# Kernel tuning notes

Hardware: AMD Instinct MI355X
Metric: run time of the kernel (lower is better)

Reference implementation:

```python
import jax, jax.numpy as jnp
import numpy as np
import math

B, S, HID, H = 2, 4096, 512, 8
D_K = HID // H


def setup_inputs() -> dict:
    key = jax.random.key(0)
    ks = jax.random.split(key, 8)
    inp = {
        "query": jax.random.normal(ks[0], (B, S, HID), dtype=jnp.float32),
        "key": jax.random.normal(ks[1], (B, S, HID), dtype=jnp.float32),
        "value": jax.random.normal(ks[2], (B, S, HID), dtype=jnp.float32),
        "mask": jax.random.randint(ks[3], (B, S), 0, 2, dtype=jnp.int32),
        # conv1d kernel_size=1, bias=False -> plain [out,in] weights (xavier-normal-ish)
        "Wq": jax.random.normal(ks[4], (HID, HID), dtype=jnp.float32) * (1.0 / math.sqrt(HID)),
        "Wk": jax.random.normal(ks[5], (HID, HID), dtype=jnp.float32) * (1.0 / math.sqrt(HID)),
        "Wv": jax.random.normal(ks[6], (HID, HID), dtype=jnp.float32) * (1.0 / math.sqrt(HID)),
        "Wo": jax.random.normal(ks[7], (HID, HID), dtype=jnp.float32) * (1.0 / math.sqrt(HID)),
    }
    return inp


def reference(query, key, value, mask, Wq, Wk, Wv, Wo):
    b, s, _ = query.shape
    # conv1d(k=1, bias=False) projection == x @ W.T; split heads -> [b,h,s,d_k]
    def proj(x, W):
        return jnp.einsum('bsd,ed->bse', x, W).reshape(b, s, H, D_K).transpose(0, 2, 1, 3)
    q, k, v = proj(query, Wq), proj(key, Wk), proj(value, Wv)
    # NOTE: original scales by 1/log(d_k), not 1/sqrt(d_k)
    score = jnp.einsum('bhqd,bhkd->bhqk', q, k) / math.log(D_K)
    m = mask.reshape(b, 1, 1, s)  # broadcast over heads and query positions
    score = jnp.where(m == 0, jnp.float32(-1e30), score)
    attn = jax.nn.softmax(score, axis=-1)  # dropout is identity in eval
    x = jnp.einsum('bhqk,bhkd->bhqd', attn, v)
    x = x.transpose(0, 2, 1, 3).reshape(b, s, HID)
    return jnp.einsum('bsd,ed->bse', x, Wo)
```

## Files before the change

### kernel.cpp

```cpp
#include <hip/hip_runtime.h>
#include <hip/hip_bf16.h>
#include <cstdint>
#include <cstddef>


namespace {

constexpr int kB = 2, kS = 4096, kHid = 512, kH = 8, kDk = 64;
constexpr int kBH = kB * kH;
constexpr int kM = kB * kS;

typedef __attribute__((ext_vector_type(8))) short short8;
typedef __attribute__((ext_vector_type(4))) float floatx4;
typedef __attribute__((ext_vector_type(16))) float floatx16;
typedef __attribute__((ext_vector_type(4))) unsigned int uintx4;
typedef unsigned short u16;

__device__ __forceinline__ u16 bf16rne(float f) {
    uint32_t u = __float_as_uint(f);
    u += 0x7fffu + ((u >> 16) & 1u);
    return (u16)(u >> 16);
}
__device__ __forceinline__ uint32_t pk2(float lo, float hi) {
#if __has_builtin(__builtin_amdgcn_cvt_pk_bf16_f32)
    typedef __attribute__((ext_vector_type(2))) __bf16 bf2;
    bf2 h = __builtin_amdgcn_cvt_pk_bf16_f32(lo, hi);
    return __builtin_bit_cast(uint32_t, h);
#else
    return ((uint32_t)bf16rne(hi) << 16) | (uint32_t)bf16rne(lo);
#endif
}
__device__ __forceinline__ float fexp2(float x) {
#if __has_builtin(__builtin_amdgcn_exp2f)
    return __builtin_amdgcn_exp2f(x);
#else
    return exp2f(x);
#endif
}
__device__ __forceinline__ float bf2f(u16 v) {
    return __uint_as_float((uint32_t)v << 16);
}
__device__ __forceinline__ void plswap(uint32_t& a, uint32_t& b) {
#if __has_builtin(__builtin_amdgcn_permlane32_swap)
    typedef __attribute__((ext_vector_type(2))) unsigned int uint2v;
    uint2v r = __builtin_amdgcn_permlane32_swap(a, b, false, false);
    a = r[0]; b = r[1];
#else
    asm volatile("v_permlane32_swap_b32 %0, %1" : "+v"(a), "+v"(b));
#endif
}
__device__ __forceinline__ void gload16(const void* g, void* l) {
    __builtin_amdgcn_global_load_lds(
        (const __attribute__((address_space(1))) void*)g,
        (__attribute__((address_space(3))) void*)l, 16, 0, 0);
}

__global__ __launch_bounds__(256) void cvt_qw(const float* __restrict__ q,
    const float* __restrict__ k, const float* __restrict__ v,
    const float* __restrict__ w0, const float* __restrict__ w1,
    const float* __restrict__ w2, const float* __restrict__ w3,
    u16* __restrict__ xall, u16* __restrict__ wall) {
    const int bx = blockIdx.x;
    if (bx < 12288) {
        int z = bx >> 12;
        size_t i = (size_t)(bx & 4095) * 256 + threadIdx.x;
        const float* src = z == 0 ? q : (z == 1 ? k : v);
        float4 f = ((const float4*)src)[i];
        ushort4 o;
        o.x = bf16rne(f.x); o.y = bf16rne(f.y);
        o.z = bf16rne(f.z); o.w = bf16rne(f.w);
        ((ushort4*)(xall + (size_t)z * kM * kHid))[i] = o;
    } else {
        int r = bx - 12288;
        int z = r >> 8;
        size_t i = (size_t)(r & 255) * 256 + threadIdx.x;
        const float* src = z == 0 ? w0 : (z == 1 ? w1 : (z == 2 ? w2 : w3));
        float sc = (z == 0)
            ? (float)(1.4426950408889634 / (6.0 * 0.6931471805599453))
            : 1.0f;
        float4 f = ((const float4*)src)[i];
        ushort4 o;
        o.x = bf16rne(f.x * sc); o.y = bf16rne(f.y * sc);
        o.z = bf16rne(f.z * sc); o.w = bf16rne(f.w * sc);
        ((ushort4*)(wall + (size_t)z * kHid * kHid))[i] = o;
    }
}

__global__ __launch_bounds__(256) void cvt_mask(const int* __restrict__ mask,
    float* __restrict__ fb) {
    int i = blockIdx.x * 256 + threadIdx.x;
    fb[i] = mask[i] ? 0.0f : -1e30f;
}

__global__ __launch_bounds__(256, 3) void proj(const u16* __restrict__ xall,
    const u16* __restrict__ wall, u16* __restrict__ qp, u16* __restrict__ kp,
    u16* __restrict__ vt) {
    __shared__ float smt[4][16][68];
    const int z = blockIdx.z;
    const u16* x = xall + (size_t)z * kM * kHid;
    const u16* w = wall + (size_t)z * kHid * kHid;
    const int wv = threadIdx.x >> 6, lane = threadIdx.x & 63;
    const int quad = lane >> 4, l16 = lane & 15;
    const int mb = blockIdx.y * 128 + (wv >> 1) * 64;
    const int nb = blockIdx.x * 128 + (wv & 1) * 64;
    floatx4 acc[4][4] = {};
    const u16* xr = x + (size_t)(mb + l16) * kHid + quad * 8;
    const u16* wr = w + (size_t)(nb + l16) * kHid + quad * 8;
    for (int k0 = 0; k0 < kHid; k0 += 32) {
        short8 a[4], bt[4];
#pragma unroll
        for (int i = 0; i < 4; i++)
            a[i] = *(const short8*)(xr + (size_t)i * 16 * kHid + k0);
#pragma unroll
        for (int t = 0; t < 4; t++)
            bt[t] = *(const short8*)(wr + (size_t)t * 16 * kHid + k0);
#pragma unroll
        for (int i = 0; i < 4; i++)
#pragma unroll
        for (int t = 0; t < 4; t++)
            acc[i][t] = __builtin_amdgcn_mfma_f32_16x16x32_bf16(a[i], bt[t], acc[i][t], 0, 0, 0);
    }
    if (z < 2) {
        u16* dst = (z == 0) ? qp : kp;
        const int row16 = lane >> 2, cseg = (lane & 3) * 16;
#pragma unroll
        for (int i = 0; i < 4; i++) {
#pragma unroll
            for (int t = 0; t < 4; t++)
#pragma unroll
            for (int r = 0; r < 4; r++)
                smt[wv][quad * 4 + r][t * 16 + l16] = acc[i][t][r];
            __builtin_amdgcn_wave_barrier();
            const float* rp = &smt[wv][row16][cseg];
            float4 f0 = *(const float4*)(rp);
            float4 f1 = *(const float4*)(rp + 4);
            float4 f2 = *(const float4*)(rp + 8);
            float4 f3 = *(const float4*)(rp + 12);
            uint4 o0, o1;
            o0.x = pk2(f0.x, f0.y); o0.y = pk2(f0.z, f0.w);
            o0.z = pk2(f1.x, f1.y); o0.w = pk2(f1.z, f1.w);
            o1.x = pk2(f2.x, f2.y); o1.y = pk2(f2.z, f2.w);
            o1.z = pk2(f3.x, f3.y); o1.w = pk2(f3.z, f3.w);
            u16* dp = dst + (size_t)(mb + i * 16 + row16) * kHid + nb + cseg;
            *(uint4*)dp = o0;
            *(uint4*)(dp + 8) = o1;
            __builtin_amdgcn_wave_barrier();
        }
    } else {
#pragma unroll
        for (int i = 0; i < 4; i++)
#pragma unroll
        for (int t = 0; t < 4; t++) {
            int m0 = mb + i * 16 + quad * 4;
            int n = nb + t * 16 + l16;
            int b = m0 >> 12, s = m0 & (kS - 1);
            int h = n >> 6,   d = n & (kDk - 1);
            ushort4 o;
            o.x = bf16rne(acc[i][t][0]); o.y = bf16rne(acc[i][t][1]);
            o.z = bf16rne(acc[i][t][2]); o.w = bf16rne(acc[i][t][3]);
            *(ushort4*)(vt + ((size_t)(b * kH + h) * kDk + d) * kS + s) = o;
        }
    }
}

__global__ __launch_bounds__(256, 2) void attn(const u16* __restrict__ qp,
    const u16* __restrict__ kp, const u16* __restrict__ vt,
    const float* __restrict__ fbias, u16* __restrict__ ows,
    float* __restrict__ rsws) {
    union SmT {
        struct { u16 K[2][64][64]; u16 V[2][64][64]; } s;
        float ep[4][32][33];
    };
    __shared__ __align__(16) SmT sm;
    const int tid = threadIdx.x;
    const int wv = tid >> 6, l = tid & 63;
    const int hf = l >> 5, q32 = l & 31, l7 = l & 7;
    const int wg = blockIdx.x;
    const int bh = ((wg & 7) << 1) | ((wg >> 3) & 1);
    const int qb = (wg >> 4) & 15;
    const int kz = wg >> 8;
    const int b = bh >> 3, h = bh & 7;
    const int qbase = qb * 256 + wv * 64;
    const u16* Qb = qp + (size_t)b * kS * kHid + h * 64;
    const u16* Kb = kp + (size_t)b * kS * kHid + h * 64;
    const u16* Vb = vt + (size_t)bh * kDk * kS;
    const float* fm = fbias + b * kS;

    short8 qf[2][4];
#pragma unroll
    for (int qt = 0; qt < 2; qt++)
#pragma unroll
    for (int m = 0; m < 4; m++)
        qf[qt][m] = *(const short8*)(Qb + (size_t)(qbase + qt * 32 + q32) * kHid + m * 16 + hf * 8);

    floatx16 O[2][2] = {};
    float rs[2] = {0.0f, 0.0f};

    const int srow = l >> 3;
    const int pcol = (l7 ^ srow) * 8;
    const u16* pK = Kb + (size_t)(kz * 64 + wv * 8 + srow) * kHid + pcol;
    const u16* pV = Vb + (size_t)(wv * 8 + srow) * kS + kz * 64 + pcol;
    auto stage = [&](int ph) {
        gload16(pK,                        &sm.s.K[ph][wv * 8][0]);
        gload16(pK + (size_t)32 * kHid,    &sm.s.K[ph][wv * 8 + 32][0]);
        gload16(pV,                        &sm.s.V[ph][wv * 8][0]);
        gload16(pV + (size_t)32 * kS,      &sm.s.V[ph][wv * 8 + 32][0]);
        pK += (size_t)128 * kHid;
        pV += 128;
    };

    stage(0);
    __syncthreads();

    for (int s5 = 0; s5 < 32; ++s5) {
        const int ph = s5 & 1;
        const int kt = (kz + 2 * s5) * 64;
        if (s5 < 31) stage(ph ^ 1);
#pragma unroll
        for (int ks = 0; ks < 2; ++ks) {
            short8 kf[4];
#pragma unroll
            for (int m = 0; m < 4; m++)
                kf[m] = *(const short8*)&sm.s.K[ph][ks * 32 + q32][((2 * m + hf) ^ l7) * 8];
            short8 vf[2][2];
#pragma unroll
            for (int ds = 0; ds < 2; ds++)
#pragma unroll
            for (int tt = 0; tt < 2; tt++)
                vf[ds][tt] = *(const short8*)&sm.s.V[ph][ds * 32 + q32][((ks * 4 + tt * 2 + hf) ^ l7) * 8];
            const float* fp = fm + kt + ks * 32 + 4 * hf;
            float4 g0 = *(const float4*)(fp);
            float4 g1 = *(const float4*)(fp + 8);
            float4 g2 = *(const float4*)(fp + 16);
            float4 g3 = *(const float4*)(fp + 24);
#pragma unroll
            for (int qt = 0; qt < 2; ++qt) {
                floatx16 st;
                st[0] = g0.x;  st[1] = g0.y;  st[2] = g0.z;  st[3] = g0.w;
                st[4] = g1.x;  st[5] = g1.y;  st[6] = g1.z;  st[7] = g1.w;
                st[8] = g2.x;  st[9] = g2.y;  st[10] = g2.z; st[11] = g2.w;
                st[12] = g3.x; st[13] = g3.y; st[14] = g3.z; st[15] = g3.w;
#pragma unroll
                for (int m = 0; m < 4; m++)
                    st = __builtin_amdgcn_mfma_f32_32x32x16_bf16(kf[m], qf[qt][m], st, 0, 0, 0);
                float xx[16];
#pragma unroll
                for (int r = 0; r < 16; r++) xx[r] = fexp2(st[r]);
                rs[qt] += (((xx[0] + xx[1]) + (xx[2] + xx[3])) + ((xx[4] + xx[5]) + (xx[6] + xx[7])))
                        + (((xx[8] + xx[9]) + (xx[10] + xx[11])) + ((xx[12] + xx[13]) + (xx[14] + xx[15])));
                uint32_t w00 = pk2(xx[0], xx[1]),   w01 = pk2(xx[2], xx[3]);
                uint32_t w10 = pk2(xx[4], xx[5]),   w11 = pk2(xx[6], xx[7]);
                uint32_t w20 = pk2(xx[8], xx[9]),   w21 = pk2(xx[10], xx[11]);
                uint32_t w30 = pk2(xx[12], xx[13]), w31 = pk2(xx[14], xx[15]);
                plswap(w00, w10); plswap(w01, w11);
                plswap(w20, w30); plswap(w21, w31);
                uintx4 t0 = {w00, w01, w10, w11};
                uintx4 t1 = {w20, w21, w30, w31};
                short8 bf0 = __builtin_bit_cast(short8, t0);
                short8 bf1 = __builtin_bit_cast(short8, t1);
                O[qt][0] = __builtin_amdgcn_mfma_f32_32x32x16_bf16(vf[0][0], bf0, O[qt][0], 0, 0, 0);
                O[qt][0] = __builtin_amdgcn_mfma_f32_32x32x16_bf16(vf[0][1], bf1, O[qt][0], 0, 0, 0);
                O[qt][1] = __builtin_amdgcn_mfma_f32_32x32x16_bf16(vf[1][0], bf0, O[qt][1], 0, 0, 0);
                O[qt][1] = __builtin_amdgcn_mfma_f32_32x32x16_bf16(vf[1][1], bf1, O[qt][1], 0, 0, 0);
            }
        }
        __syncthreads();
    }

#pragma unroll
    for (int qt = 0; qt < 2; ++qt) {
        float r = rs[qt];
        r += __shfl_xor(r, 32);
        if (hf == 0)
            rsws[((size_t)kz * kBH + bh) * kS + qbase + qt * 32 + q32] = r;
        u16* Ob = ows + (((size_t)kz * kBH + bh) * kS + qbase + qt * 32) * kDk;
#pragma unroll
        for (int ds = 0; ds < 2; ds++) {
#pragma unroll
            for (int rr = 0; rr < 16; rr++)
                sm.ep[wv][q32][(rr & 3) + 8 * (rr >> 2) + 4 * hf] = O[qt][ds][rr];
            __builtin_amdgcn_wave_barrier();
            {
                const int qq = l >> 1, c0 = (l & 1) * 16;
                float f[16];
#pragma unroll
                for (int j = 0; j < 16; j++) f[j] = sm.ep[wv][qq][c0 + j];
                uint4 o0, o1;
                o0.x = pk2(f[0], f[1]);   o0.y = pk2(f[2], f[3]);
                o0.z = pk2(f[4], f[5]);   o0.w = pk2(f[6], f[7]);
                o1.x = pk2(f[8], f[9]);   o1.y = pk2(f[10], f[11]);
                o1.z = pk2(f[12], f[13]); o1.w = pk2(f[14], f[15]);
                u16* dp = Ob + (size_t)qq * kDk + ds * 32 + c0;
                *(uint4*)dp = o0;
                *(uint4*)(dp + 8) = o1;
            }
            __builtin_amdgcn_wave_barrier();
        }
    }
}

__global__ __launch_bounds__(256) void combine(const u16* __restrict__ ows,
    const float* __restrict__ rsws, u16* __restrict__ xo) {
    size_t i = (size_t)blockIdx.x * 256 + threadIdx.x;
    const int d8 = (int)(i & 7);
    const int s  = (int)((i >> 3) & (kS - 1));
    const int bh = (int)(i >> 15);
    const int b = bh >> 3, h = bh & 7;
    const size_t base = ((size_t)bh * kS + s) * kDk + d8 * 8;
    short8 a = *(const short8*)(ows + base);
    short8 c = *(const short8*)(ows + (size_t)kBH * kS * kDk + base);
    float r = rsws[(size_t)bh * kS + s] + rsws[(size_t)kBH * kS + (size_t)bh * kS + s];
    float inv = 1.0f / r;
    float e[8];
#pragma unroll
    for (int j = 0; j < 8; j++)
        e[j] = (bf2f((u16)a[j]) + bf2f((u16)c[j])) * inv;
    uint4 o;
    o.x = pk2(e[0], e[1]); o.y = pk2(e[2], e[3]);
    o.z = pk2(e[4], e[5]); o.w = pk2(e[6], e[7]);
    *(uint4*)(xo + ((size_t)b * kS + s) * kHid + h * 64 + d8 * 8) = o;
}

__global__ __launch_bounds__(256, 3) void oproj(const u16* __restrict__ x,
    const u16* __restrict__ w, float* __restrict__ out) {
    const int wv = threadIdx.x >> 6, lane = threadIdx.x & 63;
    const int quad = lane >> 4, l16 = lane & 15;
    const int mb = blockIdx.y * 128 + (wv >> 1) * 64;
    const int nb = blockIdx.x * 128 + (wv & 1) * 64;
    floatx4 acc[4][4] = {};
    const u16* xr = x + (size_t)(mb + l16) * kHid + quad * 8;
    const u16* wr = w + (size_t)(nb + l16) * kHid + quad * 8;
    for (int k0 = 0; k0 < kHid; k0 += 32) {
        short8 a[4], bt[4];
#pragma unroll
        for (int i = 0; i < 4; i++)
            a[i] = *(const short8*)(xr + (size_t)i * 16 * kHid + k0);
#pragma unroll
        for (int t = 0; t < 4; t++)
            bt[t] = *(const short8*)(wr + (size_t)t * 16 * kHid + k0);
#pragma unroll
        for (int i = 0; i < 4; i++)
#pragma unroll
        for (int t = 0; t < 4; t++)
            acc[i][t] = __builtin_amdgcn_mfma_f32_16x16x32_bf16(a[i], bt[t], acc[i][t], 0, 0, 0);
    }
#pragma unroll
    for (int i = 0; i < 4; i++)
#pragma unroll
    for (int t = 0; t < 4; t++)
#pragma unroll
    for (int r = 0; r < 4; r++) {
        int m = mb + i * 16 + quad * 4 + r;
        int n = nb + t * 16 + l16;
        out[(size_t)m * kHid + n] = acc[i][t][r];
    }
}

}

extern "C" void kernel_launch(void* const* d_in, const int* in_sizes, int n_in,
                              void* d_out, int out_size, void* d_ws, size_t ws_size,
                              hipStream_t stream) {
    const float* q  = (const float*)d_in[0];
    const float* k  = (const float*)d_in[1];
    const float* v  = (const float*)d_in[2];
    const int* mask = (const int*)d_in[3];
    const float* w0 = (const float*)d_in[4];
    const float* w1 = (const float*)d_in[5];
    const float* w2 = (const float*)d_in[6];
    const float* w3 = (const float*)d_in[7];
    float* out = (float*)d_out;

    u16* ws   = (u16*)d_ws;
    u16* xall = ws;
    u16* wall = xall + (size_t)3 * kM * kHid;
    u16* qp   = wall + (size_t)4 * kHid * kHid;
    u16* kp   = qp + (size_t)kBH * kS * kDk;
    u16* vt   = kp + (size_t)kBH * kS * kDk;
    u16* ows  = xall;
    float* fbias = (float*)(xall + (size_t)2 * kM * kHid);
    float* rsws  = fbias + (size_t)kB * kS;
    u16* xo   = qp;

    dim3 blk(256);
    cvt_qw <<<dim3(13312), blk, 0, stream>>>(q, k, v, w0, w1, w2, w3, xall, wall);
    proj   <<<dim3(kHid / 128, kM / 128, 3), blk, 0, stream>>>(xall, wall, qp, kp, vt);
    cvt_mask<<<dim3(kB * kS / 256), blk, 0, stream>>>(mask, fbias);
    attn   <<<dim3(512), blk, 0, stream>>>(qp, kp, vt, fbias, ows, rsws);
    combine<<<dim3(2048), blk, 0, stream>>>(ows, rsws, xo);
    oproj  <<<dim3(kHid / 128, kM / 128), blk, 0, stream>>>(
        xo, wall + (size_t)3 * kHid * kHid, out);
}
```

Baseline: 264.9 us.

## Fuse fp32-to-bf16 conversion into projections and split attention keys three ways

Drops the standalone conversion kernel. The projection and output-projection GEMMs now read fp32 inputs and weights and convert them to bf16 in registers, and the softmax scale moves to the Q projection epilogue. Attention splits the key range into three partitions instead of two (768 blocks, occupancy hint raised to 3), and combine sums three partial results. This removes one launch and a bf16 round trip through memory, but each GEMM tile now loads twice as many bytes and the extra key split adds partial-output traffic. The mask loads also move inside the qt loop and the row-sum reduction uses packed float2 adds.

```diff
diff --git a/kernel.cpp b/kernel.cpp
--- a/kernel.cpp
+++ b/kernel.cpp
@@ -9,8 +9,10 @@
 constexpr int kB = 2, kS = 4096, kHid = 512, kH = 8, kDk = 64;
 constexpr int kBH = kB * kH;
 constexpr int kM = kB * kS;
+constexpr int kKZ = 3;
 
 typedef __attribute__((ext_vector_type(8))) short short8;
+typedef __attribute__((ext_vector_type(2))) float float2v;
 typedef __attribute__((ext_vector_type(4))) float floatx4;
 typedef __attribute__((ext_vector_type(16))) float floatx16;
 typedef __attribute__((ext_vector_type(4))) unsigned int uintx4;
@@ -54,36 +56,11 @@
         (const __attribute__((address_space(1))) void*)g,
         (__attribute__((address_space(3))) void*)l, 16, 0, 0);
 }
-
-__global__ __launch_bounds__(256) void cvt_qw(const float* __restrict__ q,
-    const float* __restrict__ k, const float* __restrict__ v,
-    const float* __restrict__ w0, const float* __restrict__ w1,
-    const float* __restrict__ w2, const float* __restrict__ w3,
-    u16* __restrict__ xall, u16* __restrict__ wall) {
-    const int bx = blockIdx.x;
-    if (bx < 12288) {
-        int z = bx >> 12;
-        size_t i = (size_t)(bx & 4095) * 256 + threadIdx.x;
-        const float* src = z == 0 ? q : (z == 1 ? k : v);
-        float4 f = ((const float4*)src)[i];
-        ushort4 o;
-        o.x = bf16rne(f.x); o.y = bf16rne(f.y);
-        o.z = bf16rne(f.z); o.w = bf16rne(f.w);
-        ((ushort4*)(xall + (size_t)z * kM * kHid))[i] = o;
-    } else {
-        int r = bx - 12288;
-        int z = r >> 8;
-        size_t i = (size_t)(r & 255) * 256 + threadIdx.x;
-        const float* src = z == 0 ? w0 : (z == 1 ? w1 : (z == 2 ? w2 : w3));
-        float sc = (z == 0)
-            ? (float)(1.4426950408889634 / (6.0 * 0.6931471805599453))
-            : 1.0f;
-        float4 f = ((const float4*)src)[i];
-        ushort4 o;
-        o.x = bf16rne(f.x * sc); o.y = bf16rne(f.y * sc);
-        o.z = bf16rne(f.z * sc); o.w = bf16rne(f.w * sc);
-        ((ushort4*)(wall + (size_t)z * kHid * kHid))[i] = o;
-    }
+__device__ __forceinline__ short8 cvt8(const float* p) {
+    float4 a = *(const float4*)p;
+    float4 b = *(const float4*)(p + 4);
+    uintx4 u = {pk2(a.x, a.y), pk2(a.z, a.w), pk2(b.x, b.y), pk2(b.z, b.w)};
+    return __builtin_bit_cast(short8, u);
 }
 
 __global__ __launch_bounds__(256) void cvt_mask(const int* __restrict__ mask,
@@ -92,28 +69,30 @@
     fb[i] = mask[i] ? 0.0f : -1e30f;
 }
 
-__global__ __launch_bounds__(256, 3) void proj(const u16* __restrict__ xall,
-    const u16* __restrict__ wall, u16* __restrict__ qp, u16* __restrict__ kp,
-    u16* __restrict__ vt) {
+__global__ __launch_bounds__(256, 3) void proj(const float* __restrict__ xq,
+    const float* __restrict__ xk, const float* __restrict__ xv,
+    const float* __restrict__ w0, const float* __restrict__ w1,
+    const float* __restrict__ w2,
+    u16* __restrict__ qp, u16* __restrict__ kp, u16* __restrict__ vt) {
     __shared__ float smt[4][16][68];
     const int z = blockIdx.z;
-    const u16* x = xall + (size_t)z * kM * kHid;
-    const u16* w = wall + (size_t)z * kHid * kHid;
+    const float* x = z == 0 ? xq : (z == 1 ? xk : xv);
+    const float* w = z == 0 ? w0 : (z == 1 ? w1 : w2);
     const int wv = threadIdx.x >> 6, lane = threadIdx.x & 63;
     const int quad = lane >> 4, l16 = lane & 15;
     const int mb = blockIdx.y * 128 + (wv >> 1) * 64;
     const int nb = blockIdx.x * 128 + (wv & 1) * 64;
     floatx4 acc[4][4] = {};
-    const u16* xr = x + (size_t)(mb + l16) * kHid + quad * 8;
-    const u16* wr = w + (size_t)(nb + l16) * kHid + quad * 8;
+    const float* xr = x + (size_t)(mb + l16) * kHid + quad * 8;
+    const float* wr = w + (size_t)(nb + l16) * kHid + quad * 8;
     for (int k0 = 0; k0 < kHid; k0 += 32) {
         short8 a[4], bt[4];
 #pragma unroll
         for (int i = 0; i < 4; i++)
-            a[i] = *(const short8*)(xr + (size_t)i * 16 * kHid + k0);
+            a[i] = cvt8(xr + (size_t)i * 16 * kHid + k0);
 #pragma unroll
         for (int t = 0; t < 4; t++)
-            bt[t] = *(const short8*)(wr + (size_t)t * 16 * kHid + k0);
+            bt[t] = cvt8(wr + (size_t)t * 16 * kHid + k0);
 #pragma unroll
         for (int i = 0; i < 4; i++)
 #pragma unroll
@@ -121,6 +100,8 @@
             acc[i][t] = __builtin_amdgcn_mfma_f32_16x16x32_bf16(a[i], bt[t], acc[i][t], 0, 0, 0);
     }
     if (z < 2) {
+        const float scl = (z == 0)
+            ? (float)(1.4426950408889634 / (6.0 * 0.6931471805599453)) : 1.0f;
         u16* dst = (z == 0) ? qp : kp;
         const int row16 = lane >> 2, cseg = (lane & 3) * 16;
 #pragma unroll
@@ -137,10 +118,10 @@
             float4 f2 = *(const float4*)(rp + 8);
             float4 f3 = *(const float4*)(rp + 12);
             uint4 o0, o1;
-            o0.x = pk2(f0.x, f0.y); o0.y = pk2(f0.z, f0.w);
-            o0.z = pk2(f1.x, f1.y); o0.w = pk2(f1.z, f1.w);
-            o1.x = pk2(f2.x, f2.y); o1.y = pk2(f2.z, f2.w);
-            o1.z = pk2(f3.x, f3.y); o1.w = pk2(f3.z, f3.w);
+            o0.x = pk2(f0.x * scl, f0.y * scl); o0.y = pk2(f0.z * scl, f0.w * scl);
+            o0.z = pk2(f1.x * scl, f1.y * scl); o0.w = pk2(f1.z * scl, f1.w * scl);
+            o1.x = pk2(f2.x * scl, f2.y * scl); o1.y = pk2(f2.z * scl, f2.w * scl);
+            o1.z = pk2(f3.x * scl, f3.y * scl); o1.w = pk2(f3.z * scl, f3.w * scl);
             u16* dp = dst + (size_t)(mb + i * 16 + row16) * kHid + nb + cseg;
             *(uint4*)dp = o0;
             *(uint4*)(dp + 8) = o1;
@@ -163,7 +144,7 @@
     }
 }
 
-__global__ __launch_bounds__(256, 2) void attn(const u16* __restrict__ qp,
+__global__ __launch_bounds__(256, 3) void attn(const u16* __restrict__ qp,
     const u16* __restrict__ kp, const u16* __restrict__ vt,
     const float* __restrict__ fbias, u16* __restrict__ ows,
     float* __restrict__ rsws) {
@@ -176,9 +157,13 @@
     const int wv = tid >> 6, l = tid & 63;
     const int hf = l >> 5, q32 = l & 31, l7 = l & 7;
     const int wg = blockIdx.x;
-    const int bh = ((wg & 7) << 1) | ((wg >> 3) & 1);
-    const int qb = (wg >> 4) & 15;
-    const int kz = wg >> 8;
+    const int xcd = wg & 7;
+    const int widx = wg >> 3;
+    const int bh = (xcd << 1) | (widx & 1);
+    const int rest = widx >> 1;
+    const int qb = rest & 15;
+    const int kz = rest >> 4;
+    const int nt = (kz == 0) ? 22 : 21;
     const int b = bh >> 3, h = bh & 7;
     const int qbase = qb * 256 + wv * 64;
     const u16* Qb = qp + (size_t)b * kS * kHid + h * 64;
@@ -205,17 +190,17 @@
         gload16(pK + (size_t)32 * kHid,    &sm.s.K[ph][wv * 8 + 32][0]);
         gload16(pV,                        &sm.s.V[ph][wv * 8][0]);
         gload16(pV + (size_t)32 * kS,      &sm.s.V[ph][wv * 8 + 32][0]);
-        pK += (size_t)128 * kHid;
-        pV += 128;
+        pK += (size_t)(kKZ * 64) * kHid;
+        pV += kKZ * 64;
     };
 
     stage(0);
     __syncthreads();
 
-    for (int s5 = 0; s5 < 32; ++s5) {
+    for (int s5 = 0; s5 < nt; ++s5) {
         const int ph = s5 & 1;
-        const int kt = (kz + 2 * s5) * 64;
-        if (s5 < 31) stage(ph ^ 1);
+        const int kt = (kz + kKZ * s5) * 64;
+        if (s5 < nt - 1) stage(ph ^ 1);
 #pragma unroll
         for (int ks = 0; ks < 2; ++ks) {
             short8 kf[4];
@@ -229,12 +214,12 @@
             for (int tt = 0; tt < 2; tt++)
                 vf[ds][tt] = *(const short8*)&sm.s.V[ph][ds * 32 + q32][((ks * 4 + tt * 2 + hf) ^ l7) * 8];
             const float* fp = fm + kt + ks * 32 + 4 * hf;
-            float4 g0 = *(const float4*)(fp);
-            float4 g1 = *(const float4*)(fp + 8);
-            float4 g2 = *(const float4*)(fp + 16);
-            float4 g3 = *(const float4*)(fp + 24);
 #pragma unroll
             for (int qt = 0; qt < 2; ++qt) {
+                float4 g0 = *(const float4*)(fp);
+                float4 g1 = *(const float4*)(fp + 8);
+                float4 g2 = *(const float4*)(fp + 16);
+                float4 g3 = *(const float4*)(fp + 24);
                 floatx16 st;
                 st[0] = g0.x;  st[1] = g0.y;  st[2] = g0.z;  st[3] = g0.w;
                 st[4] = g1.x;  st[5] = g1.y;  st[6] = g1.z;  st[7] = g1.w;
@@ -246,8 +231,14 @@
                 float xx[16];
 #pragma unroll
                 for (int r = 0; r < 16; r++) xx[r] = fexp2(st[r]);
-                rs[qt] += (((xx[0] + xx[1]) + (xx[2] + xx[3])) + ((xx[4] + xx[5]) + (xx[6] + xx[7])))
-                        + (((xx[8] + xx[9]) + (xx[10] + xx[11])) + ((xx[12] + xx[13]) + (xx[14] + xx[15])));
+                float2v a0 = {xx[0], xx[1]},  a1 = {xx[2], xx[3]};
+                float2v a2 = {xx[4], xx[5]},  a3 = {xx[6], xx[7]};
+                float2v a4 = {xx[8], xx[9]},  a5 = {xx[10], xx[11]};
+                float2v a6 = {xx[12], xx[13]}, a7 = {xx[14], xx[15]};
+                a0 += a1; a2 += a3; a4 += a5; a6 += a7;
+                a0 += a2; a4 += a6;
+                a0 += a4;
+                rs[qt] += a0[0] + a0[1];
                 uint32_t w00 = pk2(xx[0], xx[1]),   w01 = pk2(xx[2], xx[3]);
                 uint32_t w10 = pk2(xx[4], xx[5]),   w11 = pk2(xx[6], xx[7]);
                 uint32_t w20 = pk2(xx[8], xx[9]),   w21 = pk2(xx[10], xx[11]);
@@ -307,14 +298,18 @@
     const int bh = (int)(i >> 15);
     const int b = bh >> 3, h = bh & 7;
     const size_t base = ((size_t)bh * kS + s) * kDk + d8 * 8;
-    short8 a = *(const short8*)(ows + base);
-    short8 c = *(const short8*)(ows + (size_t)kBH * kS * kDk + base);
-    float r = rsws[(size_t)bh * kS + s] + rsws[(size_t)kBH * kS + (size_t)bh * kS + s];
+    const size_t kzs = (size_t)kBH * kS * kDk;
+    short8 a0 = *(const short8*)(ows + base);
+    short8 a1 = *(const short8*)(ows + kzs + base);
+    short8 a2 = *(const short8*)(ows + 2 * kzs + base);
+    float r = rsws[(size_t)bh * kS + s]
+            + rsws[(size_t)kBH * kS + (size_t)bh * kS + s]
+            + rsws[(size_t)2 * kBH * kS + (size_t)bh * kS + s];
     float inv = 1.0f / r;
     float e[8];
 #pragma unroll
     for (int j = 0; j < 8; j++)
-        e[j] = (bf2f((u16)a[j]) + bf2f((u16)c[j])) * inv;
+        e[j] = (bf2f((u16)a0[j]) + bf2f((u16)a1[j]) + bf2f((u16)a2[j])) * inv;
     uint4 o;
     o.x = pk2(e[0], e[1]); o.y = pk2(e[2], e[3]);
     o.z = pk2(e[4], e[5]); o.w = pk2(e[6], e[7]);
@@ -322,14 +317,14 @@
 }
 
 __global__ __launch_bounds__(256, 3) void oproj(const u16* __restrict__ x,
-    const u16* __restrict__ w, float* __restrict__ out) {
+    const float* __restrict__ w, float* __restrict__ out) {
     const int wv = threadIdx.x >> 6, lane = threadIdx.x & 63;
     const int quad = lane >> 4, l16 = lane & 15;
     const int mb = blockIdx.y * 128 + (wv >> 1) * 64;
     const int nb = blockIdx.x * 128 + (wv & 1) * 64;
     floatx4 acc[4][4] = {};
     const u16* xr = x + (size_t)(mb + l16) * kHid + quad * 8;
-    const u16* wr = w + (size_t)(nb + l16) * kHid + quad * 8;
+    const float* wr = w + (size_t)(nb + l16) * kHid + quad * 8;
     for (int k0 = 0; k0 < kHid; k0 += 32) {
         short8 a[4], bt[4];
 #pragma unroll
@@ -337,7 +332,7 @@
             a[i] = *(const short8*)(xr + (size_t)i * 16 * kHid + k0);
 #pragma unroll
         for (int t = 0; t < 4; t++)
-            bt[t] = *(const short8*)(wr + (size_t)t * 16 * kHid + k0);
+            bt[t] = cvt8(wr + (size_t)t * 16 * kHid + k0);
 #pragma unroll
         for (int i = 0; i < 4; i++)
 #pragma unroll
@@ -372,22 +367,21 @@
     float* out = (float*)d_out;
 
     u16* ws   = (u16*)d_ws;
-    u16* xall = ws;
-    u16* wall = xall + (size_t)3 * kM * kHid;
-    u16* qp   = wall + (size_t)4 * kHid * kHid;
+    u16* regA = ws;
+    u16* regB = regA + (size_t)3 * kM * kHid;
+    u16* qp   = regB + (size_t)4 * kHid * kHid;
     u16* kp   = qp + (size_t)kBH * kS * kDk;
     u16* vt   = kp + (size_t)kBH * kS * kDk;
-    u16* ows  = xall;
-    float* fbias = (float*)(xall + (size_t)2 * kM * kHid);
+    u16* ows  = regA;
+    float* fbias = (float*)regB;
     float* rsws  = fbias + (size_t)kB * kS;
     u16* xo   = qp;
 
     dim3 blk(256);
-    cvt_qw <<<dim3(13312), blk, 0, stream>>>(q, k, v, w0, w1, w2, w3, xall, wall);
-    proj   <<<dim3(kHid / 128, kM / 128, 3), blk, 0, stream>>>(xall, wall, qp, kp, vt);
     cvt_mask<<<dim3(kB * kS / 256), blk, 0, stream>>>(mask, fbias);
-    attn   <<<dim3(512), blk, 0, stream>>>(qp, kp, vt, fbias, ows, rsws);
+    proj   <<<dim3(kHid / 128, kM / 128, 3), blk, 0, stream>>>(q, k, v, w0, w1, w2,
+                                                               qp, kp, vt);
+    attn   <<<dim3(768), blk, 0, stream>>>(qp, kp, vt, fbias, ows, rsws);
     combine<<<dim3(2048), blk, 0, stream>>>(ows, rsws, xo);
-    oproj  <<<dim3(kHid / 128, kM / 128), blk, 0, stream>>>(
-        xo, wall + (size_t)3 * kHid * kHid, out);
-}
+    oproj  <<<dim3(kHid / 128, kM / 128), blk, 0, stream>>>(xo, w3, out);
+}
```

Result: slower. 365.7 us (+38.1%).
